# Kernel optimization log

Hardware: AMD Instinct MI355X
Metric: run time of the kernel (lower is better)

## Reference

```python
import jax, jax.numpy as jnp
import numpy as np

H, DH, C = 16, 64, 1024  # num_head, head_size, embed_size
B, T = 4, 2048

def setup_inputs() -> dict:
    key = jax.random.key(0)
    ks = jax.random.split(key, 6)
    s = 1.0 / np.sqrt(C)
    x  = jax.random.normal(ks[0], (B, T, C), dtype=jnp.float32)
    # per-head projection weights, stacked: [H, C, DH] (PyTorch Linear computes x @ W.T; we store W.T directly)
    Wq = jax.random.uniform(ks[1], (H, C, DH), dtype=jnp.float32, minval=-s, maxval=s)
    Wk = jax.random.uniform(ks[2], (H, C, DH), dtype=jnp.float32, minval=-s, maxval=s)
    Wv = jax.random.uniform(ks[3], (H, C, DH), dtype=jnp.float32, minval=-s, maxval=s)
    Wo = jax.random.uniform(ks[4], (C, C), dtype=jnp.float32, minval=-s, maxval=s)
    bo = jax.random.uniform(ks[5], (C,), dtype=jnp.float32, minval=-s, maxval=s)
    return {"x": x, "Wq": Wq, "Wk": Wk, "Wv": Wv, "Wo": Wo, "bo": bo}

def reference(x, Wq, Wk, Wv, Wo, bo):
    # Dropout layers act as identity (eval mode).
    q = jnp.einsum('btc,hcd->bhtd', x, Wq)
    k = jnp.einsum('btc,hcd->bhtd', x, Wk)
    v = jnp.einsum('btc,hcd->bhtd', x, Wv)
    scale = 1.0 / np.sqrt(DH).astype(np.float32)
    wei = jnp.einsum('bhtd,bhsd->bhts', q, k) * scale  # [B,H,T,T]
    Tn = x.shape[1]
    causal = jnp.tril(jnp.ones((Tn, Tn), dtype=bool))
    wei = jnp.where(causal, wei, -jnp.inf)
    wei = jax.nn.softmax(wei, axis=-1)
    out = jnp.einsum('bhts,bhsd->bhtd', wei, v)  # [B,H,T,DH]
    out = out.transpose(0, 2, 1, 3).reshape(x.shape[0], Tn, H * DH)  # concat heads
    return out @ Wo + bo
```

## Files before the change

kernel.cpp:

```cpp
#include <hip/hip_runtime.h>
#include <hip/hip_bf16.h>

typedef __attribute__((ext_vector_type(8))) short short8;
typedef __attribute__((ext_vector_type(4))) short s4v;
typedef __attribute__((ext_vector_type(4))) float floatx4;

static constexpr int Hn = 16, DHn = 64, Cn = 1024;
static constexpr int Bn = 4, Tn = 2048;
static constexpr int Mtot = Bn * Tn;
static constexpr size_t QKV_STRIDE = (size_t)Bn * Hn * Tn * DHn;

__device__ __forceinline__ unsigned short bfbits(float f) {
    __hip_bfloat16 h = __float2bfloat16(f);
    return __builtin_bit_cast(unsigned short, h);
}

__device__ __forceinline__ void gl_lds16(const void* g, void* lds_base) {
    __builtin_amdgcn_global_load_lds(
        (const __attribute__((address_space(1))) unsigned int*)g,
        (__attribute__((address_space(3))) unsigned int*)lds_base, 16, 0, 0);
}

__global__ void conv_kernel(const float4* __restrict__ src, ushort4* __restrict__ dst, int n4) {
    int i = blockIdx.x * blockDim.x + threadIdx.x;
    if (i < n4) {
        float4 v = src[i];
        ushort4 o;
        o.x = bfbits(v.x); o.y = bfbits(v.y); o.z = bfbits(v.z); o.w = bfbits(v.w);
        dst[i] = o;
    }
}

__global__ void tconv_kernel(const float* __restrict__ src, __hip_bfloat16* __restrict__ dst,
                             int R, int C, float scale) {
    __shared__ float tile[32][33];
    const float* s = src + (size_t)blockIdx.z * R * C;
    __hip_bfloat16* d = dst + (size_t)blockIdx.z * R * C;
    int c0 = blockIdx.x * 32;
    int r0 = blockIdx.y * 32;
    int tx = threadIdx.x;
    int ty = threadIdx.y;
    for (int i = 0; i < 4; ++i) {
        int r = r0 + ty + i * 8;
        tile[ty + i * 8][tx] = s[(size_t)r * C + c0 + tx];
    }
    __syncthreads();
    for (int i = 0; i < 4; ++i) {
        int c = c0 + ty + i * 8;
        d[(size_t)c * R + r0 + tx] = __float2bfloat16(tile[tx][ty + i * 8] * scale);
    }
}

template<int MODE>
__global__ __launch_bounds__(256) void gemm_kernel(
    const __hip_bfloat16* __restrict__ A,
    const __hip_bfloat16* __restrict__ BT,
    const float* __restrict__ bias,
    __hip_bfloat16* __restrict__ out_qkv,
    float* __restrict__ out_f32)
{
    constexpr int K = Cn;
    __shared__ __hip_bfloat16 lA[128 * 64];
    __shared__ __hip_bfloat16 lB[128 * 64];
    const int m0 = blockIdx.x * 128;
    const int n0 = blockIdx.y * 128;
    const int tid = threadIdx.x;
    const int lane = tid & 63, wid = tid >> 6;
    const int wy = wid >> 1, wx = wid & 1;
    const int fr = lane & 15, g = lane >> 4;
    const int rxor = (fr & 7) << 4;
    char* const lA0 = (char*)lA;
    char* const lB0 = (char*)lB;

    floatx4 acc[4][4] = {};

    int srow[4], scol[4], dbase[4];
#pragma unroll
    for (int i = 0; i < 4; ++i) {
        int byteoff = wid * 4096 + i * 1024 + lane * 16;
        int r = byteoff >> 7;
        int ch = (byteoff >> 4) & 7;
        srow[i] = r;
        scol[i] = (ch ^ (r & 7)) << 3;
        dbase[i] = wid * 4096 + i * 1024;
    }

    for (int k0 = 0; k0 < K; k0 += 64) {
#pragma unroll
        for (int i = 0; i < 4; ++i) {
            gl_lds16(&A[(size_t)(m0 + srow[i]) * K + k0 + scol[i]], lA0 + dbase[i]);
            gl_lds16(&BT[(size_t)(n0 + srow[i]) * K + k0 + scol[i]], lB0 + dbase[i]);
        }
        asm volatile("s_waitcnt vmcnt(0)" ::: "memory");
        __syncthreads();
#pragma unroll
        for (int kk = 0; kk < 2; ++kk) {
            short8 af[4], bf[4];
#pragma unroll
            for (int t = 0; t < 4; ++t) {
                af[t] = *(const short8*)(lA0 + (wy * 64 + t * 16 + fr) * 128 + ((kk * 64 + g * 16) ^ rxor));
                bf[t] = *(const short8*)(lB0 + (wx * 64 + t * 16 + fr) * 128 + ((kk * 64 + g * 16) ^ rxor));
            }
#pragma unroll
            for (int tm = 0; tm < 4; ++tm)
#pragma unroll
                for (int tn = 0; tn < 4; ++tn)
                    acc[tm][tn] = __builtin_amdgcn_mfma_f32_16x16x32_bf16(af[tm], bf[tn], acc[tm][tn], 0, 0, 0);
        }
        __syncthreads();
    }

    for (int tm = 0; tm < 4; ++tm) {
        int rbase = m0 + wy * 64 + tm * 16 + g * 4;
        for (int tn = 0; tn < 4; ++tn) {
            int nc = n0 + wx * 64 + tn * 16 + fr;
            if (MODE == 0) {
                int w = nc >> 10, rem = nc & 1023, hh = rem >> 6, dd = rem & 63;
                if (w == 2) {
                    int b = rbase >> 11, t0 = rbase & 2047;
                    ushort4 pk;
                    pk.x = bfbits(acc[tm][tn][0]);
                    pk.y = bfbits(acc[tm][tn][1]);
                    pk.z = bfbits(acc[tm][tn][2]);
                    pk.w = bfbits(acc[tm][tn][3]);
                    *(ushort4*)(&out_qkv[2 * QKV_STRIDE +
                        ((size_t)((b * Hn + hh) * DHn + dd)) * Tn + t0]) = pk;
                } else {
                    for (int r = 0; r < 4; ++r) {
                        int m = rbase + r;
                        int b = m >> 11, t = m & 2047;
                        out_qkv[(size_t)w * QKV_STRIDE + (((size_t)(b * Hn + hh) * Tn + t) << 6) + dd] =
                            __float2bfloat16(acc[tm][tn][r]);
                    }
                }
            } else {
                float bs = bias[nc];
                for (int r = 0; r < 4; ++r) {
                    int m = rbase + r;
                    out_f32[(size_t)m * Cn + nc] = acc[tm][tn][r] + bs;
                }
            }
        }
    }
}

__global__ __launch_bounds__(256) void attn_kernel(
    const __hip_bfloat16* __restrict__ q,
    const __hip_bfloat16* __restrict__ k,
    const __hip_bfloat16* __restrict__ vt,
    __hip_bfloat16* __restrict__ ao)
{
    __shared__ char smem[65536];

    const int id = blockIdx.x;
    const int bh = (id & 7) * 8 + ((id >> 3) & 7);
    const int p = id >> 6;
    const int b = bh >> 4, h = bh & 15;
    const int tid = threadIdx.x, lane = tid & 63, wid = tid >> 6;
    const int fr = lane & 15, g = lane >> 4;
    const size_t base = (size_t)bh * Tn * DHn;
    const int rxor = (fr & 7) << 4;

    const int r0 = wid * 16 + (lane >> 3);
    const int c8 = ((lane & 7) ^ (r0 & 7)) * 8;
    const int ldk0 = wid * 2048;

    short8 ones;
#pragma unroll
    for (int z = 0; z < 8; ++z) ones[z] = (short)0x3F80;

    const int tiles[2] = { 15 - p, p };

    for (int tt = 0; tt < 2; ++tt) {
        const int qb0 = tiles[tt] * 128;
        const int q0 = qb0 + wid * 32;
        const int nkv = qb0 / 64 + 2;

        short8 aq[2][2];
#pragma unroll
        for (int rq = 0; rq < 2; ++rq)
#pragma unroll
            for (int kk = 0; kk < 2; ++kk)
                aq[rq][kk] = *(const short8*)(&q[base + (size_t)(q0 + rq * 16 + fr) * DHn + kk * 32 + g * 8]);

        floatx4 o[2][4] = {};
        floatx4 o5[2] = {};

#pragma unroll
        for (int jj = 0; jj < 2; ++jj) {
            char* kd = smem + jj * 8192 + ldk0;
            char* vd = smem + 32768 + jj * 8192 + ldk0;
            const int v0 = jj * 64;
            gl_lds16(&k[base + (size_t)(v0 + r0) * DHn + c8], kd);
            gl_lds16(&k[base + (size_t)(v0 + r0 + 8) * DHn + c8], kd + 1024);
            gl_lds16(&vt[base + (size_t)r0 * Tn + v0 + c8], vd);
            gl_lds16(&vt[base + (size_t)(r0 + 8) * Tn + v0 + c8], vd + 1024);
        }

        for (int j = 0; j < nkv; ++j) {
            const int kv0 = j * 64;
            const int cur = j & 3;
            {
                const int bi = (j + 2) & 3;
                const int nv0 = kv0 + 128;
                char* kd = smem + bi * 8192 + ldk0;
                char* vd = smem + 32768 + bi * 8192 + ldk0;
                gl_lds16(&k[base + (size_t)(nv0 + r0) * DHn + c8], kd);
                gl_lds16(&k[base + (size_t)(nv0 + r0 + 8) * DHn + c8], kd + 1024);
                gl_lds16(&vt[base + (size_t)r0 * Tn + nv0 + c8], vd);
                gl_lds16(&vt[base + (size_t)(r0 + 8) * Tn + nv0 + c8], vd + 1024);
            }
            asm volatile("s_waitcnt vmcnt(8)" ::: "memory");
            __builtin_amdgcn_s_barrier();

            if (kv0 < q0 + 32) {
                const char* lkc = smem + cur * 8192;
                const char* lvc = smem + 32768 + cur * 8192;

                floatx4 s[2][4] = {};
                __builtin_amdgcn_s_setprio(1);
#pragma unroll
                for (int kk = 0; kk < 2; ++kk)
#pragma unroll
                    for (int cg = 0; cg < 4; ++cg) {
                        short8 kf = *(const short8*)(lkc + (cg * 16 + fr) * 128 + ((g * 16 + kk * 64) ^ rxor));
                        s[0][cg] = __builtin_amdgcn_mfma_f32_16x16x32_bf16(kf, aq[0][kk], s[0][cg], 0, 0, 0);
                        s[1][cg] = __builtin_amdgcn_mfma_f32_16x16x32_bf16(kf, aq[1][kk], s[1][cg], 0, 0, 0);
                    }
                __builtin_amdgcn_s_setprio(0);

                if (kv0 + 64 > q0) {
#pragma unroll
                    for (int rq = 0; rq < 2; ++rq) {
                        int qg = q0 + rq * 16 + fr;
#pragma unroll
                        for (int cg = 0; cg < 4; ++cg) {
                            int kg = kv0 + cg * 16 + g * 4;
#pragma unroll
                            for (int r = 0; r < 4; ++r)
                                if (kg + r > qg) s[rq][cg][r] = -1e30f;
                        }
                    }
                }

                short8 pb[2][2];
#pragma unroll
                for (int rq = 0; rq < 2; ++rq) {
#pragma unroll
                    for (int cg = 0; cg < 4; ++cg)
#pragma unroll
                        for (int r = 0; r < 4; ++r)
                            s[rq][cg][r] = __builtin_amdgcn_exp2f(s[rq][cg][r]);
#pragma unroll
                    for (int kt = 0; kt < 2; ++kt) {
                        short8 pk;
#pragma unroll
                        for (int r = 0; r < 4; ++r) {
                            pk[r]     = (short)bfbits(s[rq][2 * kt][r]);
                            pk[r + 4] = (short)bfbits(s[rq][2 * kt + 1][r]);
                        }
                        pb[rq][kt] = pk;
                    }
                }

                __builtin_amdgcn_s_setprio(1);
#pragma unroll
                for (int rq = 0; rq < 2; ++rq)
#pragma unroll
                    for (int kt = 0; kt < 2; ++kt)
                        o5[rq] = __builtin_amdgcn_mfma_f32_16x16x32_bf16(ones, pb[rq][kt], o5[rq], 0, 0, 0);
#pragma unroll
                for (int kt = 0; kt < 2; ++kt)
#pragma unroll
                    for (int dg = 0; dg < 4; ++dg) {
                        const int vrow = (dg * 16 + fr) * 128;
                        s4v lo = *(const s4v*)(lvc + vrow + ((kt * 64 + 8 * g) ^ rxor));
                        s4v hi = *(const s4v*)(lvc + vrow + ((kt * 64 + 32 + 8 * g) ^ rxor));
                        short8 vf = __builtin_shufflevector(lo, hi, 0, 1, 2, 3, 4, 5, 6, 7);
                        o[0][dg] = __builtin_amdgcn_mfma_f32_16x16x32_bf16(vf, pb[0][kt], o[0][dg], 0, 0, 0);
                        o[1][dg] = __builtin_amdgcn_mfma_f32_16x16x32_bf16(vf, pb[1][kt], o[1][dg], 0, 0, 0);
                    }
                __builtin_amdgcn_s_setprio(0);
            }
        }

        asm volatile("s_waitcnt vmcnt(0)" ::: "memory");
        __syncthreads();

        char* myscr = smem + wid * 4096;
        const int rr = lane >> 2, cc = lane & 3;
#pragma unroll
        for (int rq = 0; rq < 2; ++rq) {
            const float inv = 1.0f / o5[rq][0];
#pragma unroll
            for (int dg = 0; dg < 4; ++dg) {
                floatx4 wv = o[rq][dg] * inv;
                *(floatx4*)(myscr + fr * 256 + ((dg * 64 + g * 16) ^ rxor)) = wv;
            }
            asm volatile("s_waitcnt lgkmcnt(0)" ::: "memory");
            float4 f0 = *(const float4*)(myscr + rr * 256 + ((cc * 64 + 0) ^ ((rr & 7) << 4)));
            float4 f1 = *(const float4*)(myscr + rr * 256 + ((cc * 64 + 16) ^ ((rr & 7) << 4)));
            float4 f2 = *(const float4*)(myscr + rr * 256 + ((cc * 64 + 32) ^ ((rr & 7) << 4)));
            float4 f3 = *(const float4*)(myscr + rr * 256 + ((cc * 64 + 48) ^ ((rr & 7) << 4)));
            short8 pk0, pk1;
            pk0[0] = (short)bfbits(f0.x); pk0[1] = (short)bfbits(f0.y);
            pk0[2] = (short)bfbits(f0.z); pk0[3] = (short)bfbits(f0.w);
            pk0[4] = (short)bfbits(f1.x); pk0[5] = (short)bfbits(f1.y);
            pk0[6] = (short)bfbits(f1.z); pk0[7] = (short)bfbits(f1.w);
            pk1[0] = (short)bfbits(f2.x); pk1[1] = (short)bfbits(f2.y);
            pk1[2] = (short)bfbits(f2.z); pk1[3] = (short)bfbits(f2.w);
            pk1[4] = (short)bfbits(f3.x); pk1[5] = (short)bfbits(f3.y);
            pk1[6] = (short)bfbits(f3.z); pk1[7] = (short)bfbits(f3.w);
            size_t orow = ((size_t)(b * Tn + q0 + rq * 16 + rr)) * Cn + h * 64 + cc * 16;
            *(short8*)(&ao[orow]) = pk0;
            *(short8*)(&ao[orow + 8]) = pk1;
            asm volatile("s_waitcnt lgkmcnt(0)" ::: "memory");
        }
        __syncthreads();
    }
}

extern "C" void kernel_launch(void* const* d_in, const int* in_sizes, int n_in,
                              void* d_out, int out_size, void* d_ws, size_t ws_size,
                              hipStream_t stream) {
    const float* x  = (const float*)d_in[0];
    const float* Wq = (const float*)d_in[1];
    const float* Wk = (const float*)d_in[2];
    const float* Wv = (const float*)d_in[3];
    const float* Wo = (const float*)d_in[4];
    const float* bo = (const float*)d_in[5];
    float* out = (float*)d_out;

    char* ws = (char*)d_ws;
    __hip_bfloat16* xb  = (__hip_bfloat16*)(ws);
    __hip_bfloat16* wT  = (__hip_bfloat16*)(ws + 16777216);
    __hip_bfloat16* woT = (__hip_bfloat16*)(ws + 23068672);
    __hip_bfloat16* qb  = (__hip_bfloat16*)(ws + 25165824);
    __hip_bfloat16* ao  = (__hip_bfloat16*)(ws + 75497472);

    conv_kernel<<<(Mtot * Cn / 4 + 255) / 256, 256, 0, stream>>>(
        (const float4*)x, (ushort4*)xb, Mtot * Cn / 4);
    tconv_kernel<<<dim3(2, 32, 16), dim3(32, 8), 0, stream>>>(Wq, wT + 0 * 1048576, Cn, DHn, 0.125f * 1.44269504088896f);
    tconv_kernel<<<dim3(2, 32, 16), dim3(32, 8), 0, stream>>>(Wk, wT + 1 * 1048576, Cn, DHn, 1.0f);
    tconv_kernel<<<dim3(2, 32, 16), dim3(32, 8), 0, stream>>>(Wv, wT + 2 * 1048576, Cn, DHn, 1.0f);
    tconv_kernel<<<dim3(32, 32, 1), dim3(32, 8), 0, stream>>>(Wo, woT, Cn, Cn, 1.0f);

    gemm_kernel<0><<<dim3(Mtot / 128, 3072 / 128), 256, 0, stream>>>(
        xb, wT, nullptr, qb, nullptr);

    attn_kernel<<<dim3(512), 256, 0, stream>>>(
        qb, qb + QKV_STRIDE, qb + 2 * QKV_STRIDE, ao);

    gemm_kernel<1><<<dim3(Mtot / 128, Cn / 128), 256, 0, stream>>>(
        ao, woT, bo, nullptr, out);
}
```

Baseline: 168.2 us.

## Double-buffer GEMM LDS tiles with async prefetch and swizzled block order

The GEMM kernel now uses two LDS stages, issuing global-to-LDS loads for the next K step before running MFMAs on the current one. This overlaps memory latency with compute instead of waiting on every step. It also remaps a 1D grid with an 8-way swizzle for better L2 reuse and raises wave priority around the MFMA block. LDS use doubles to 64KB per block, which may lower occupancy.

```diff
diff --git a/kernel.cpp b/kernel.cpp
--- a/kernel.cpp
+++ b/kernel.cpp
@@ -60,21 +60,24 @@
     float* __restrict__ out_f32)
 {
     constexpr int K = Cn;
-    __shared__ __hip_bfloat16 lA[128 * 64];
-    __shared__ __hip_bfloat16 lB[128 * 64];
-    const int m0 = blockIdx.x * 128;
-    const int n0 = blockIdx.y * 128;
+    constexpr int NSTEP = K / 64;
+    __shared__ char smem[65536];
+
+    const int cpx = gridDim.x >> 3;
+    const int bid = blockIdx.x;
+    const int swz = (bid & 7) * cpx + (bid >> 3);
+    const int m0 = (swz & 63) * 128;
+    const int n0 = (swz >> 6) * 128;
+
     const int tid = threadIdx.x;
     const int lane = tid & 63, wid = tid >> 6;
     const int wy = wid >> 1, wx = wid & 1;
     const int fr = lane & 15, g = lane >> 4;
     const int rxor = (fr & 7) << 4;
-    char* const lA0 = (char*)lA;
-    char* const lB0 = (char*)lB;
 
     floatx4 acc[4][4] = {};
 
-    int srow[4], scol[4], dbase[4];
+    int srow[4], scol[4], doff[4];
 #pragma unroll
     for (int i = 0; i < 4; ++i) {
         int byteoff = wid * 4096 + i * 1024 + lane * 16;
@@ -82,32 +85,49 @@
         int ch = (byteoff >> 4) & 7;
         srow[i] = r;
         scol[i] = (ch ^ (r & 7)) << 3;
-        dbase[i] = wid * 4096 + i * 1024;
-    }
-
-    for (int k0 = 0; k0 < K; k0 += 64) {
-#pragma unroll
-        for (int i = 0; i < 4; ++i) {
-            gl_lds16(&A[(size_t)(m0 + srow[i]) * K + k0 + scol[i]], lA0 + dbase[i]);
-            gl_lds16(&BT[(size_t)(n0 + srow[i]) * K + k0 + scol[i]], lB0 + dbase[i]);
-        }
-        asm volatile("s_waitcnt vmcnt(0)" ::: "memory");
-        __syncthreads();
+        doff[i] = wid * 4096 + i * 1024;
+    }
+
+#pragma unroll
+    for (int i = 0; i < 4; ++i) {
+        gl_lds16(&A[(size_t)(m0 + srow[i]) * K + scol[i]], smem + doff[i]);
+        gl_lds16(&BT[(size_t)(n0 + srow[i]) * K + scol[i]], smem + 16384 + doff[i]);
+    }
+    asm volatile("s_waitcnt vmcnt(0)" ::: "memory");
+    asm volatile("s_barrier" ::: "memory");
+
+    int cur = 0;
+    for (int t = 0; t < NSTEP; ++t) {
+        if (t + 1 < NSTEP) {
+            const int k0 = (t + 1) * 64;
+            char* dst = smem + (cur ^ 1) * 32768;
+#pragma unroll
+            for (int i = 0; i < 4; ++i) {
+                gl_lds16(&A[(size_t)(m0 + srow[i]) * K + k0 + scol[i]], dst + doff[i]);
+                gl_lds16(&BT[(size_t)(n0 + srow[i]) * K + k0 + scol[i]], dst + 16384 + doff[i]);
+            }
+        }
+        const char* lA0 = smem + cur * 32768;
+        const char* lB0 = lA0 + 16384;
 #pragma unroll
         for (int kk = 0; kk < 2; ++kk) {
             short8 af[4], bf[4];
 #pragma unroll
-            for (int t = 0; t < 4; ++t) {
-                af[t] = *(const short8*)(lA0 + (wy * 64 + t * 16 + fr) * 128 + ((kk * 64 + g * 16) ^ rxor));
-                bf[t] = *(const short8*)(lB0 + (wx * 64 + t * 16 + fr) * 128 + ((kk * 64 + g * 16) ^ rxor));
-            }
+            for (int t4 = 0; t4 < 4; ++t4) {
+                af[t4] = *(const short8*)(lA0 + (wy * 64 + t4 * 16 + fr) * 128 + ((kk * 64 + g * 16) ^ rxor));
+                bf[t4] = *(const short8*)(lB0 + (wx * 64 + t4 * 16 + fr) * 128 + ((kk * 64 + g * 16) ^ rxor));
+            }
+            __builtin_amdgcn_s_setprio(1);
 #pragma unroll
             for (int tm = 0; tm < 4; ++tm)
 #pragma unroll
                 for (int tn = 0; tn < 4; ++tn)
                     acc[tm][tn] = __builtin_amdgcn_mfma_f32_16x16x32_bf16(af[tm], bf[tn], acc[tm][tn], 0, 0, 0);
-        }
-        __syncthreads();
+            __builtin_amdgcn_s_setprio(0);
+        }
+        asm volatile("s_waitcnt vmcnt(0)" ::: "memory");
+        asm volatile("s_barrier" ::: "memory");
+        cur ^= 1;
     }
 
     for (int tm = 0; tm < 4; ++tm) {
@@ -345,12 +365,12 @@
     tconv_kernel<<<dim3(2, 32, 16), dim3(32, 8), 0, stream>>>(Wv, wT + 2 * 1048576, Cn, DHn, 1.0f);
     tconv_kernel<<<dim3(32, 32, 1), dim3(32, 8), 0, stream>>>(Wo, woT, Cn, Cn, 1.0f);
 
-    gemm_kernel<0><<<dim3(Mtot / 128, 3072 / 128), 256, 0, stream>>>(
+    gemm_kernel<0><<<dim3(1536), 256, 0, stream>>>(
         xb, wT, nullptr, qb, nullptr);
 
     attn_kernel<<<dim3(512), 256, 0, stream>>>(
         qb, qb + QKV_STRIDE, qb + 2 * QKV_STRIDE, ao);
 
-    gemm_kernel<1><<<dim3(Mtot / 128, Cn / 128), 256, 0, stream>>>(
+    gemm_kernel<1><<<dim3(512), 256, 0, stream>>>(
         ao, woT, bo, nullptr, out);
 }
```

Measured after the change: 176.0 us. +4.7%, slower.
